# Optimization experiments

Hardware: AMD Instinct MI355X
Metric: run time of the kernel (lower is better)

The kernel has to match this reference:

```python
import jax, jax.numpy as jnp
import numpy as np

EPS = 1e-5
ALPHA = 0.7
N_HEADS = 20
N_KV_HEADS = 5
HEAD_DIM = 128


def bitlinear(x, w):
    # absmean ternary quantization per output row: w_t = sign(w)*(|w| > alpha*absmean)
    absw = jnp.abs(w)
    absmean = jnp.mean(absw, axis=1, keepdims=True)            # [out, 1]
    tern = jnp.sign(w) * (absw > ALPHA * absmean).astype(w.dtype)
    # (X @ pos^T - X @ neg^T) * scale == (X @ tern^T) * scale
    return jnp.einsum('...i,oi->...o', x, tern) * absmean[:, 0]


def rmsnorm(x, g):
    var = jnp.mean(jnp.square(x), axis=-1, keepdims=True)
    return x * jax.lax.rsqrt(var + EPS) * g


def rotate_half(x):
    x1, x2 = jnp.split(x, 2, axis=-1)
    return jnp.concatenate([-x2, x1], axis=-1)


def setup_inputs() -> dict:
    key = jax.random.key(0)
    ks = jax.random.split(key, 12)
    h, inter = 2560, 6912
    b, s = 1, 2048
    wscale = 1.0 / np.sqrt(h)
    return {
        'x': jax.random.normal(ks[0], (b, s, h), jnp.float32),
        'cos': jax.random.uniform(ks[1], (1, 1, s, HEAD_DIM), jnp.float32),
        'sin': jax.random.uniform(ks[2], (1, 1, s, HEAD_DIM), jnp.float32),
        'q_w': jax.random.normal(ks[3], (h, h), jnp.float32) * wscale,
        'k_w': jax.random.normal(ks[4], (N_KV_HEADS * HEAD_DIM, h), jnp.float32) * wscale,
        'v_w': jax.random.normal(ks[5], (N_KV_HEADS * HEAD_DIM, h), jnp.float32) * wscale,
        'o_w': jax.random.normal(ks[6], (h, h), jnp.float32) * wscale,
        'gate_w': jax.random.normal(ks[7], (inter, h), jnp.float32) * wscale,
        'up_w': jax.random.normal(ks[8], (inter, h), jnp.float32) * wscale,
        'down_w': jax.random.normal(ks[9], (h, inter), jnp.float32) / np.sqrt(inter),
        'ln1_w': jnp.ones((h,), jnp.float32),
        'ln2_w': jnp.ones((h,), jnp.float32),
    }


def reference(x, cos, sin, q_w, k_w, v_w, o_w, gate_w, up_w, down_w, ln1_w, ln2_w):
    b, s, hdim = x.shape
    residual = x
    h = rmsnorm(x, ln1_w)

    q = bitlinear(h, q_w).reshape(b, s, N_HEADS, HEAD_DIM).transpose(0, 2, 1, 3)
    k = bitlinear(h, k_w).reshape(b, s, N_KV_HEADS, HEAD_DIM).transpose(0, 2, 1, 3)
    v = bitlinear(h, v_w).reshape(b, s, N_KV_HEADS, HEAD_DIM).transpose(0, 2, 1, 3)

    # RoPE
    q = q * cos + rotate_half(q) * sin
    k = k * cos + rotate_half(k) * sin

    # GQA: repeat_interleave kv heads
    n_rep = N_HEADS // N_KV_HEADS
    k = jnp.repeat(k, n_rep, axis=1)
    v = jnp.repeat(v, n_rep, axis=1)

    scale = 1.0 / np.sqrt(HEAD_DIM)
    attn = jnp.einsum('bhqd,bhkd->bhqk', q, k) * scale
    attn = jax.nn.softmax(attn, axis=-1)
    o = jnp.einsum('bhqk,bhkd->bhqd', attn, v)
    o = o.transpose(0, 2, 1, 3).reshape(b, s, hdim)

    x = residual + bitlinear(o, o_w)

    residual = x
    h = rmsnorm(x, ln2_w)
    gate = jnp.square(jax.nn.relu(bitlinear(h, gate_w)))  # relu^2
    x = residual + bitlinear(gate * bitlinear(h, up_w), down_w)
    return x
```

## Files before the change

### kernel.cpp

```cpp
#include <hip/hip_runtime.h>
#include <hip/hip_bf16.h>

typedef unsigned short u16;
typedef short bf16x8 __attribute__((ext_vector_type(8)));
typedef float f32x4 __attribute__((ext_vector_type(4)));

__device__ __forceinline__ u16 f2b(float f) {
    union { __hip_bfloat16 h; u16 u; } cv;
    cv.h = __float2bfloat16(f);
    return cv.u;
}
__device__ __forceinline__ float b2f(u16 u) {
    union { u16 u; __hip_bfloat16 h; } cv;
    cv.u = u;
    return __bfloat162float(cv.h);
}

__device__ __forceinline__ void g2l16(const void* g, void* l) {
    __builtin_amdgcn_global_load_lds(
        (const __attribute__((address_space(1))) unsigned int*)g,
        (__attribute__((address_space(3))) unsigned int*)l, 16, 0, 0);
}

template <int EPT>
__global__ __launch_bounds__(256) void quant_kernel(const float* __restrict__ W,
                                                    u16* __restrict__ T,
                                                    float* __restrict__ scales, int K) {
    const int row = blockIdx.x, tid = threadIdx.x;
    const float* wr = W + (size_t)row * K;
    float v[EPT];
    float s = 0.f;
#pragma unroll
    for (int i = 0; i < EPT; ++i) { v[i] = wr[tid + i * 256]; s += fabsf(v[i]); }
#pragma unroll
    for (int d = 1; d < 64; d <<= 1) s += __shfl_xor(s, d);
    __shared__ float red[4];
    if ((tid & 63) == 0) red[tid >> 6] = s;
    __syncthreads();
    const float absmean = (red[0] + red[1] + red[2] + red[3]) / (float)K;
    const float thr = 0.7f * absmean;
    u16* tr = T + (size_t)row * K;
#pragma unroll
    for (int i = 0; i < EPT; ++i) {
        float w = v[i];
        float t = (fabsf(w) > thr) ? ((w > 0.f) ? 1.f : -1.f) : 0.f;
        tr[tid + i * 256] = f2b(t);
    }
    if (tid == 0) scales[row] = absmean;
}

__global__ __launch_bounds__(256) void rmsnorm_kernel(const float* __restrict__ x,
                                                      const float* __restrict__ g,
                                                      u16* __restrict__ o) {
    const int row = blockIdx.x, tid = threadIdx.x;
    const float* xr = x + (size_t)row * 2560;
    float v[10];
    float s = 0.f;
#pragma unroll
    for (int i = 0; i < 10; ++i) { v[i] = xr[tid + i * 256]; s += v[i] * v[i]; }
#pragma unroll
    for (int d = 1; d < 64; d <<= 1) s += __shfl_xor(s, d);
    __shared__ float red[4];
    if ((tid & 63) == 0) red[tid >> 6] = s;
    __syncthreads();
    const float total = red[0] + red[1] + red[2] + red[3];
    const float rs = rsqrtf(total * (1.f / 2560.f) + 1e-5f);
    u16* orow = o + (size_t)row * 2560;
#pragma unroll
    for (int i = 0; i < 10; ++i) orow[tid + i * 256] = f2b(v[i] * rs * g[tid + i * 256]);
}

template <int MODE>
__global__ __launch_bounds__(512, 4) void gemm_bt(const u16* __restrict__ A,
                                                  const u16* __restrict__ B,
                                                  const float* __restrict__ scale,
                                                  const float* __restrict__ res,
                                                  void* __restrict__ outp,
                                                  int M, int N, int K) {
    __shared__ __align__(16) u16 sA[128 * 64];
    __shared__ __align__(16) u16 sB[128 * 64];
    const int tid = threadIdx.x;
    const int wave = tid >> 6, lane = tid & 63;
    const int lane15 = lane & 15, quad = lane >> 4;
    const int m0 = blockIdx.x * 128, n0 = blockIdx.y * 128;
    const int wm = wave >> 2, wn = wave & 3;

    f32x4 acc[4][2] = {};

    const int r0 = wave * 8 + (lane >> 3);
    const int gcc = (lane & 7) ^ (lane >> 3);
    const size_t aoff = (size_t)(m0 + r0) * K + gcc * 8;
    const size_t boff = (size_t)(n0 + r0) * K + gcc * 8;
    char* ldsA = (char*)sA + wave * 1024;
    char* ldsB = (char*)sB + wave * 1024;
    const int sw = lane15 & 7;

    for (int kt = 0; kt < K; kt += 64) {
        g2l16(A + aoff + kt, ldsA);
        g2l16(A + aoff + (size_t)64 * K + kt, ldsA + 8192);
        g2l16(B + boff + kt, ldsB);
        g2l16(B + boff + (size_t)64 * K + kt, ldsB + 8192);
        __syncthreads();
#pragma unroll
        for (int kc = 0; kc < 2; ++kc) {
            const int pc = ((kc * 4 + quad) ^ sw) * 8;
            bf16x8 af[4], bfr[2];
#pragma unroll
            for (int f = 0; f < 4; ++f)
                af[f] = *(const bf16x8*)&sA[(wm * 64 + f * 16 + lane15) * 64 + pc];
#pragma unroll
            for (int f = 0; f < 2; ++f)
                bfr[f] = *(const bf16x8*)&sB[(wn * 32 + f * 16 + lane15) * 64 + pc];
#pragma unroll
            for (int i = 0; i < 4; ++i)
#pragma unroll
                for (int j = 0; j < 2; ++j)
                    acc[i][j] = __builtin_amdgcn_mfma_f32_16x16x32_bf16(af[i], bfr[j], acc[i][j], 0, 0, 0);
        }
        __syncthreads();
    }

#pragma unroll
    for (int j = 0; j < 2; ++j) {
        const int c = n0 + wn * 32 + j * 16 + lane15;
        const float sc = scale[c];
#pragma unroll
        for (int i = 0; i < 4; ++i) {
            const int rbase = m0 + wm * 64 + i * 16 + quad * 4;
#pragma unroll
            for (int r = 0; r < 4; ++r) {
                const float vv = acc[i][j][r] * sc;
                const size_t idx = (size_t)(rbase + r) * N + c;
                if (MODE == 0) ((u16*)outp)[idx] = f2b(vv);
                else           ((float*)outp)[idx] = res[idx] + vv;
            }
        }
    }
}

__global__ __launch_bounds__(256) void rope_kernel(u16* __restrict__ buf, int stride,
                                                   const float* __restrict__ cs,
                                                   const float* __restrict__ sn, int nh) {
    const int idx = blockIdx.x * 256 + threadIdx.x;
    const int d = idx & 63;
    const int h = (idx >> 6) % nh;
    const int s = idx / (64 * nh);
    const size_t base = (size_t)s * stride + h * 128;
    const float a = b2f(buf[base + d]), b = b2f(buf[base + d + 64]);
    const float c1 = cs[s * 128 + d], s1 = sn[s * 128 + d];
    const float c2 = cs[s * 128 + d + 64], s2 = sn[s * 128 + d + 64];
    buf[base + d] = f2b(a * c1 - b * s1);
    buf[base + d + 64] = f2b(b * c2 + a * s2);
}

__global__ __launch_bounds__(256) void transpose_v_kernel(const u16* __restrict__ V, int stride,
                                                          u16* __restrict__ VT) {
    __shared__ u16 t[128 * 66];
    const int tid = threadIdx.x;
    const int h = blockIdx.y, s0 = blockIdx.x * 64;
#pragma unroll
    for (int i = 0; i < 32; ++i) {
        const int idx = tid + i * 256;
        const int r = idx >> 7, c = idx & 127;
        t[c * 66 + r] = V[(size_t)(s0 + r) * stride + h * 128 + c];
    }
    __syncthreads();
#pragma unroll
    for (int i = 0; i < 32; ++i) {
        const int idx = tid + i * 256;
        const int d = idx >> 6, s = idx & 63;
        VT[((size_t)h * 128 + d) * 2048 + s0 + s] = t[d * 66 + s];
    }
}

__global__ __launch_bounds__(256, 3) void flash_kernel(const u16* __restrict__ Q, int qs,
                                                       const u16* __restrict__ Kb,
                                                       const u16* __restrict__ VT,
                                                       u16* __restrict__ O) {
    __shared__ __align__(16) u16 sQ[64 * 128];
    __shared__ __align__(16) u16 sK[64 * 128];
    __shared__ __align__(16) u16 sV[128 * 64];
    const int tid = threadIdx.x, wave = tid >> 6, lane = tid & 63;
    const int lane15 = lane & 15, quad = lane >> 4;
    const int head = blockIdx.y, q0 = blockIdx.x * 64, kvh = head >> 2;
    const int sw = lane15 & 7;

    {
        const int rq = wave * 4 + (lane >> 4);
        const int gq = (lane & 15) ^ (rq & 7);
        const u16* src = Q + (size_t)(q0 + rq) * qs + head * 128 + gq * 8;
        char* dst = (char*)sQ + wave * 1024;
#pragma unroll
        for (int s = 0; s < 4; ++s)
            g2l16(src + (size_t)s * 16 * qs, dst + s * 4096);
    }
    __syncthreads();
    bf16x8 qf[4];
#pragma unroll
    for (int kc = 0; kc < 4; ++kc)
        qf[kc] = *(const bf16x8*)&sQ[(wave * 16 + lane15) * 128 + ((kc * 4 + quad) ^ sw) * 8];

    float m_i[4], l_i[4];
    f32x4 o_acc[8] = {};
#pragma unroll
    for (int r = 0; r < 4; ++r) { m_i[r] = -1e30f; l_i[r] = 0.f; }

    const float sl2e = 0.088388347648318447f * 1.4426950408889634f;

    const int rk = wave * 4 + (lane >> 4);
    const int gk = (lane & 15) ^ (rk & 7);
    const u16* kbase = Kb + (size_t)rk * qs + kvh * 128 + gk * 8;
    const int rv = wave * 8 + (lane >> 3);
    const int gv = (lane & 7) ^ (rv & 7);
    const u16* vbase = VT + ((size_t)kvh * 128 + rv) * 2048 + gv * 8;
    char* dstK = (char*)sK + wave * 1024;
    char* dstV = (char*)sV + wave * 1024;
    u16* sP = sQ;

    for (int k0 = 0; k0 < 2048; k0 += 64) {
#pragma unroll
        for (int s = 0; s < 4; ++s) {
            g2l16(kbase + ((size_t)k0 + s * 16) * qs, dstK + s * 4096);
            g2l16(vbase + (size_t)s * 32 * 2048 + k0, dstV + s * 4096);
        }
        __syncthreads();

        f32x4 sacc[4] = {};
#pragma unroll
        for (int nf = 0; nf < 4; ++nf)
#pragma unroll
            for (int kc = 0; kc < 4; ++kc) {
                const bf16x8 kf = *(const bf16x8*)&sK[(nf * 16 + lane15) * 128 + ((kc * 4 + quad) ^ sw) * 8];
                sacc[nf] = __builtin_amdgcn_mfma_f32_16x16x32_bf16(qf[kc], kf, sacc[nf], 0, 0, 0);
            }

#pragma unroll
        for (int r = 0; r < 4; ++r) {
            float v0 = sacc[0][r] * sl2e, v1 = sacc[1][r] * sl2e;
            float v2 = sacc[2][r] * sl2e, v3 = sacc[3][r] * sl2e;
            float mx = fmaxf(fmaxf(v0, v1), fmaxf(v2, v3));
#pragma unroll
            for (int d = 1; d < 16; d <<= 1) mx = fmaxf(mx, __shfl_xor(mx, d));
            const float mnew = fmaxf(m_i[r], mx);
            const float alpha = exp2f(m_i[r] - mnew);
            m_i[r] = mnew;
            const float p0 = exp2f(v0 - mnew), p1 = exp2f(v1 - mnew);
            const float p2 = exp2f(v2 - mnew), p3 = exp2f(v3 - mnew);
            sacc[0][r] = p0; sacc[1][r] = p1; sacc[2][r] = p2; sacc[3][r] = p3;
            float sum = (p0 + p1) + (p2 + p3);
#pragma unroll
            for (int d = 1; d < 16; d <<= 1) sum += __shfl_xor(sum, d);
            l_i[r] = l_i[r] * alpha + sum;
#pragma unroll
            for (int nf = 0; nf < 8; ++nf) o_acc[nf][r] *= alpha;
        }

#pragma unroll
        for (int nf = 0; nf < 4; ++nf) {
            const int cc = nf * 2 + (lane15 >> 3);
            const int pcol = ((cc ^ quad) * 8) + (lane15 & 7);
#pragma unroll
            for (int r = 0; r < 4; ++r)
                sP[(wave * 16 + quad * 4 + r) * 64 + pcol] = f2b(sacc[nf][r]);
        }

        bf16x8 pf[2];
#pragma unroll
        for (int kc = 0; kc < 2; ++kc)
            pf[kc] = *(const bf16x8*)&sP[(wave * 16 + lane15) * 64 + ((kc * 4 + quad) ^ ((lane15 >> 2) & 3)) * 8];
#pragma unroll
        for (int nf = 0; nf < 8; ++nf)
#pragma unroll
            for (int kc = 0; kc < 2; ++kc) {
                const bf16x8 vf = *(const bf16x8*)&sV[(nf * 16 + lane15) * 64 + ((kc * 4 + quad) ^ sw) * 8];
                o_acc[nf] = __builtin_amdgcn_mfma_f32_16x16x32_bf16(pf[kc], vf, o_acc[nf], 0, 0, 0);
            }
        __syncthreads();
    }

#pragma unroll
    for (int r = 0; r < 4; ++r) {
        const float inv = 1.f / l_i[r];
        const int row = q0 + wave * 16 + quad * 4 + r;
        u16* orow = O + (size_t)row * 2560 + head * 128;
#pragma unroll
        for (int nf = 0; nf < 8; ++nf)
            orow[nf * 16 + lane15] = f2b(o_acc[nf][r] * inv);
    }
}

__global__ __launch_bounds__(256) void glu_kernel(u16* __restrict__ g, const u16* __restrict__ u) {
    const size_t i = ((size_t)blockIdx.x * 256 + threadIdx.x) * 8;
    bf16x8 gv = *(const bf16x8*)(g + i);
    bf16x8 uv = *(const bf16x8*)(u + i);
    bf16x8 ov;
#pragma unroll
    for (int j = 0; j < 8; ++j) {
        float x = b2f((u16)gv[j]);
        x = fmaxf(x, 0.f);
        ov[j] = (short)f2b(x * x * b2f((u16)uv[j]));
    }
    *(bf16x8*)(g + i) = ov;
}

extern "C" void kernel_launch(void* const* d_in, const int* in_sizes, int n_in,
                              void* d_out, int out_size, void* d_ws, size_t ws_size,
                              hipStream_t stream) {
    (void)in_sizes; (void)n_in; (void)out_size; (void)ws_size;
    const float* x      = (const float*)d_in[0];
    const float* cosb   = (const float*)d_in[1];
    const float* sinb   = (const float*)d_in[2];
    const float* q_w    = (const float*)d_in[3];
    const float* k_w    = (const float*)d_in[4];
    const float* v_w    = (const float*)d_in[5];
    const float* o_w    = (const float*)d_in[6];
    const float* gate_w = (const float*)d_in[7];
    const float* up_w   = (const float*)d_in[8];
    const float* down_w = (const float*)d_in[9];
    const float* ln1    = (const float*)d_in[10];
    const float* ln2    = (const float*)d_in[11];

    char* w = (char*)d_ws;
    size_t off = 0;
    auto nxt = [&](size_t sz) { char* p = w + off; off += sz; return p; };
    u16*   TQ = (u16*)nxt(13107200);
    u16*   TK = (u16*)nxt(3276800);
    u16*   TV = (u16*)nxt(3276800);
    u16*   TO = (u16*)nxt(13107200);
    u16*   TB = (u16*)nxt(35389440);
    float* SC = (float*)nxt(91136);
    u16*   H  = (u16*)nxt(10485760);
    u16*   QKV = (u16*)nxt(15728640);
    u16*   VT = (u16*)nxt(2621440);
    float* XM = (float*)nxt(20971520);
    u16*   G  = (u16*)nxt(28311552);
    u16*   U  = TQ;

    quant_kernel<10><<<2560, 256, 0, stream>>>(q_w, TQ, SC + 0, 2560);
    quant_kernel<10><<<640, 256, 0, stream>>>(k_w, TK, SC + 2560, 2560);
    quant_kernel<10><<<640, 256, 0, stream>>>(v_w, TV, SC + 3200, 2560);
    quant_kernel<10><<<2560, 256, 0, stream>>>(o_w, TO, SC + 3840, 2560);
    rmsnorm_kernel<<<2048, 256, 0, stream>>>(x, ln1, H);
    gemm_bt<0><<<dim3(16, 30), 512, 0, stream>>>(H, TQ, SC + 0, nullptr, QKV, 2048, 3840, 2560);
    rope_kernel<<<10240, 256, 0, stream>>>(QKV, 3840, cosb, sinb, 20);
    rope_kernel<<<2560, 256, 0, stream>>>(QKV + 2560, 3840, cosb, sinb, 5);
    transpose_v_kernel<<<dim3(32, 5), 256, 0, stream>>>(QKV + 3200, 3840, VT);
    flash_kernel<<<dim3(32, 20), 256, 0, stream>>>(QKV, 3840, QKV + 2560, VT, H);
    gemm_bt<1><<<dim3(16, 20), 512, 0, stream>>>(H, TO, SC + 3840, x, XM, 2048, 2560, 2560);

    rmsnorm_kernel<<<2048, 256, 0, stream>>>(XM, ln2, H);
    quant_kernel<10><<<6912, 256, 0, stream>>>(gate_w, TB, SC + 6400, 2560);
    gemm_bt<0><<<dim3(16, 54), 512, 0, stream>>>(H, TB, SC + 6400, nullptr, G, 2048, 6912, 2560);
    quant_kernel<10><<<6912, 256, 0, stream>>>(up_w, TB, SC + 13312, 2560);
    gemm_bt<0><<<dim3(16, 54), 512, 0, stream>>>(H, TB, SC + 13312, nullptr, U, 2048, 6912, 2560);
    glu_kernel<<<6912, 256, 0, stream>>>(G, U);
    quant_kernel<27><<<2560, 256, 0, stream>>>(down_w, TB, SC + 20224, 6912);
    gemm_bt<1><<<dim3(16, 20), 512, 0, stream>>>(G, TB, SC + 20224, XM, (float*)d_out, 2048, 2560, 6912);
}
```

Baseline: 860.9 us.

## Double-buffer K/V tiles in flash attention and skip unneeded softmax rescales

After: 885.7 us. 1.03x slower.

```diff
diff --git a/kernel.cpp b/kernel.cpp
--- a/kernel.cpp
+++ b/kernel.cpp
@@ -173,39 +173,17 @@
     }
 }
 
-__global__ __launch_bounds__(256, 3) void flash_kernel(const u16* __restrict__ Q, int qs,
+__global__ __launch_bounds__(256, 2) void flash_kernel(const u16* __restrict__ Q, int qs,
                                                        const u16* __restrict__ Kb,
                                                        const u16* __restrict__ VT,
                                                        u16* __restrict__ O) {
     __shared__ __align__(16) u16 sQ[64 * 128];
-    __shared__ __align__(16) u16 sK[64 * 128];
-    __shared__ __align__(16) u16 sV[128 * 64];
+    __shared__ __align__(16) u16 sK[2][64 * 128];
+    __shared__ __align__(16) u16 sV[2][128 * 64];
     const int tid = threadIdx.x, wave = tid >> 6, lane = tid & 63;
     const int lane15 = lane & 15, quad = lane >> 4;
     const int head = blockIdx.y, q0 = blockIdx.x * 64, kvh = head >> 2;
     const int sw = lane15 & 7;
-
-    {
-        const int rq = wave * 4 + (lane >> 4);
-        const int gq = (lane & 15) ^ (rq & 7);
-        const u16* src = Q + (size_t)(q0 + rq) * qs + head * 128 + gq * 8;
-        char* dst = (char*)sQ + wave * 1024;
-#pragma unroll
-        for (int s = 0; s < 4; ++s)
-            g2l16(src + (size_t)s * 16 * qs, dst + s * 4096);
-    }
-    __syncthreads();
-    bf16x8 qf[4];
-#pragma unroll
-    for (int kc = 0; kc < 4; ++kc)
-        qf[kc] = *(const bf16x8*)&sQ[(wave * 16 + lane15) * 128 + ((kc * 4 + quad) ^ sw) * 8];
-
-    float m_i[4], l_i[4];
-    f32x4 o_acc[8] = {};
-#pragma unroll
-    for (int r = 0; r < 4; ++r) { m_i[r] = -1e30f; l_i[r] = 0.f; }
-
-    const float sl2e = 0.088388347648318447f * 1.4426950408889634f;
 
     const int rk = wave * 4 + (lane >> 4);
     const int gk = (lane & 15) ^ (rk & 7);
@@ -213,46 +191,86 @@
     const int rv = wave * 8 + (lane >> 3);
     const int gv = (lane & 7) ^ (rv & 7);
     const u16* vbase = VT + ((size_t)kvh * 128 + rv) * 2048 + gv * 8;
-    char* dstK = (char*)sK + wave * 1024;
-    char* dstV = (char*)sV + wave * 1024;
+
+    auto stage = [&](int k0, int b) {
+        char* dK = (char*)(&sK[b][0]) + wave * 1024;
+        char* dV = (char*)(&sV[b][0]) + wave * 1024;
+#pragma unroll
+        for (int s = 0; s < 4; ++s) {
+            g2l16(kbase + ((size_t)k0 + s * 16) * qs, dK + s * 4096);
+            g2l16(vbase + (size_t)s * 32 * 2048 + k0, dV + s * 4096);
+        }
+    };
+
+    {
+        const int rq = wave * 4 + (lane >> 4);
+        const int gq = (lane & 15) ^ (rq & 7);
+        const u16* src = Q + (size_t)(q0 + rq) * qs + head * 128 + gq * 8;
+        char* dst = (char*)sQ + wave * 1024;
+#pragma unroll
+        for (int s = 0; s < 4; ++s)
+            g2l16(src + (size_t)s * 16 * qs, dst + s * 4096);
+        stage(0, 0);
+    }
+    __syncthreads();
+    bf16x8 qf[4];
+#pragma unroll
+    for (int kc = 0; kc < 4; ++kc)
+        qf[kc] = *(const bf16x8*)&sQ[(wave * 16 + lane15) * 128 + ((kc * 4 + quad) ^ sw) * 8];
+
+    float m_i[4], lp[4];
+    f32x4 o_acc[8] = {};
+#pragma unroll
+    for (int r = 0; r < 4; ++r) { m_i[r] = -1e30f; lp[r] = 0.f; }
+
+    const float sl2e = 0.088388347648318447f * 1.4426950408889634f;
     u16* sP = sQ;
 
-    for (int k0 = 0; k0 < 2048; k0 += 64) {
-#pragma unroll
-        for (int s = 0; s < 4; ++s) {
-            g2l16(kbase + ((size_t)k0 + s * 16) * qs, dstK + s * 4096);
-            g2l16(vbase + (size_t)s * 32 * 2048 + k0, dstV + s * 4096);
-        }
-        __syncthreads();
+    for (int t = 0; t < 32; ++t) {
+        const int buf = t & 1;
+        if (t < 31) stage((t + 1) * 64, buf ^ 1);
+        const u16* sKb = &sK[buf][0];
+        const u16* sVb = &sV[buf][0];
 
         f32x4 sacc[4] = {};
 #pragma unroll
         for (int nf = 0; nf < 4; ++nf)
 #pragma unroll
             for (int kc = 0; kc < 4; ++kc) {
-                const bf16x8 kf = *(const bf16x8*)&sK[(nf * 16 + lane15) * 128 + ((kc * 4 + quad) ^ sw) * 8];
+                const bf16x8 kf = *(const bf16x8*)&sKb[(nf * 16 + lane15) * 128 + ((kc * 4 + quad) ^ sw) * 8];
                 sacc[nf] = __builtin_amdgcn_mfma_f32_16x16x32_bf16(qf[kc], kf, sacc[nf], 0, 0, 0);
             }
 
+        float mx[4];
 #pragma unroll
         for (int r = 0; r < 4; ++r) {
             float v0 = sacc[0][r] * sl2e, v1 = sacc[1][r] * sl2e;
             float v2 = sacc[2][r] * sl2e, v3 = sacc[3][r] * sl2e;
-            float mx = fmaxf(fmaxf(v0, v1), fmaxf(v2, v3));
-#pragma unroll
-            for (int d = 1; d < 16; d <<= 1) mx = fmaxf(mx, __shfl_xor(mx, d));
-            const float mnew = fmaxf(m_i[r], mx);
-            const float alpha = exp2f(m_i[r] - mnew);
-            m_i[r] = mnew;
-            const float p0 = exp2f(v0 - mnew), p1 = exp2f(v1 - mnew);
-            const float p2 = exp2f(v2 - mnew), p3 = exp2f(v3 - mnew);
+            sacc[0][r] = v0; sacc[1][r] = v1; sacc[2][r] = v2; sacc[3][r] = v3;
+            float m0 = fmaxf(fmaxf(v0, v1), fmaxf(v2, v3));
+#pragma unroll
+            for (int d = 1; d < 16; d <<= 1) m0 = fmaxf(m0, __shfl_xor(m0, d));
+            mx[r] = m0;
+        }
+        const int upd = (mx[0] > m_i[0]) | (mx[1] > m_i[1]) | (mx[2] > m_i[2]) | (mx[3] > m_i[3]);
+        if (__any(upd)) {
+#pragma unroll
+            for (int r = 0; r < 4; ++r) {
+                const float mnew = fmaxf(m_i[r], mx[r]);
+                const float alpha = exp2f(m_i[r] - mnew);
+                m_i[r] = mnew;
+                lp[r] *= alpha;
+#pragma unroll
+                for (int nf = 0; nf < 8; ++nf) o_acc[nf][r] *= alpha;
+            }
+        }
+#pragma unroll
+        for (int r = 0; r < 4; ++r) {
+            const float m = m_i[r];
+            const float p0 = exp2f(sacc[0][r] - m), p1 = exp2f(sacc[1][r] - m);
+            const float p2 = exp2f(sacc[2][r] - m), p3 = exp2f(sacc[3][r] - m);
             sacc[0][r] = p0; sacc[1][r] = p1; sacc[2][r] = p2; sacc[3][r] = p3;
-            float sum = (p0 + p1) + (p2 + p3);
-#pragma unroll
-            for (int d = 1; d < 16; d <<= 1) sum += __shfl_xor(sum, d);
-            l_i[r] = l_i[r] * alpha + sum;
-#pragma unroll
-            for (int nf = 0; nf < 8; ++nf) o_acc[nf][r] *= alpha;
+            lp[r] += (p0 + p1) + (p2 + p3);
         }
 
 #pragma unroll
@@ -261,18 +279,18 @@
             const int pcol = ((cc ^ quad) * 8) + (lane15 & 7);
 #pragma unroll
             for (int r = 0; r < 4; ++r)
-                sP[(wave * 16 + quad * 4 + r) * 64 + pcol] = f2b(sacc[nf][r]);
+                sP[(wave * 16 + quad * 4 + r) * 72 + pcol] = f2b(sacc[nf][r]);
         }
 
         bf16x8 pf[2];
 #pragma unroll
         for (int kc = 0; kc < 2; ++kc)
-            pf[kc] = *(const bf16x8*)&sP[(wave * 16 + lane15) * 64 + ((kc * 4 + quad) ^ ((lane15 >> 2) & 3)) * 8];
+            pf[kc] = *(const bf16x8*)&sP[(wave * 16 + lane15) * 72 + ((kc * 4 + quad) ^ ((lane15 >> 2) & 3)) * 8];
 #pragma unroll
         for (int nf = 0; nf < 8; ++nf)
 #pragma unroll
             for (int kc = 0; kc < 2; ++kc) {
-                const bf16x8 vf = *(const bf16x8*)&sV[(nf * 16 + lane15) * 64 + ((kc * 4 + quad) ^ sw) * 8];
+                const bf16x8 vf = *(const bf16x8*)&sVb[(nf * 16 + lane15) * 64 + ((kc * 4 + quad) ^ sw) * 8];
                 o_acc[nf] = __builtin_amdgcn_mfma_f32_16x16x32_bf16(pf[kc], vf, o_acc[nf], 0, 0, 0);
             }
         __syncthreads();
@@ -280,7 +298,10 @@
 
 #pragma unroll
     for (int r = 0; r < 4; ++r) {
-        const float inv = 1.f / l_i[r];
+        float lt = lp[r];
+#pragma unroll
+        for (int d = 1; d < 16; d <<= 1) lt += __shfl_xor(lt, d);
+        const float inv = 1.f / lt;
         const int row = q0 + wave * 16 + quad * 4 + r;
         u16* orow = O + (size_t)row * 2560 + head * 128;
 #pragma unroll
```
